# Kernel tuning notes

Measured on AMD Instinct MI355X. Metric: run time of the kernel, lower is better.

The kernel has to match this reference:

```python
import jax, jax.numpy as jnp
import numpy as np

NUM_HEADS = 16
NHID = 64
D = NUM_HEADS * NHID  # 1024, also keys/query/values dim and out_dim
SL, BS = 2048, 32


def setup_inputs() -> dict:
    key = jax.random.key(0)
    ks = jax.random.split(key, 7)
    s = 1.0 / np.sqrt(D)
    return {
        "query": jax.random.normal(ks[0], (BS, D), jnp.float32),
        "keys": jax.random.normal(ks[1], (SL, BS, D), jnp.float32),
        "values": jax.random.normal(ks[2], (SL, BS, D), jnp.float32),
        "Wq": jax.random.normal(ks[3], (D, D), jnp.float32) * s,
        "Wk": jax.random.normal(ks[4], (D, D), jnp.float32) * s,
        "Wv": jax.random.normal(ks[5], (D, D), jnp.float32) * s,
        "Wo": jax.random.normal(ks[6], (D, D), jnp.float32) * s,
    }


def reference(query, keys, values, Wq, Wk, Wv, Wo):
    sl, bs, _ = keys.shape
    qp = query @ Wq.T                       # [bs, H*nhid]
    kp = keys @ Wk.T                        # [sl, bs, H*nhid]
    vp = values @ Wv.T                      # [sl, bs, H*nhid]
    # elementwise multiplicative score, reduced per head
    dot = (qp * kp).reshape(sl, bs, NUM_HEADS, NHID).sum(-1) / np.sqrt(NHID)
    # NOTE: original uses log_softmax (not softmax) over the sequence dim
    w = jax.nn.log_softmax(dot, axis=0)[..., None]        # [sl, bs, H, 1]
    attn = (w * vp.reshape(sl, bs, NUM_HEADS, NHID)).sum(0)  # [bs, H, nhid]
    return attn.reshape(bs, -1) @ Wo.T                     # [bs, D]
```

## Files before the change

### kernel.cpp

```cpp
#include <hip/hip_runtime.h>

#define SL  2048
#define BSZ 32
#define DIM 1024
#define NH  16
#define HD  64

typedef __attribute__((ext_vector_type(4))) float f32x4;
typedef __attribute__((ext_vector_type(8))) short s16x8;

static __device__ __forceinline__ short f2bf(float f) {
    union { float f; unsigned u; } v; v.f = f;
    unsigned r = (v.u + 0x7fffu + ((v.u >> 16) & 1u)) >> 16;
    return (short)r;
}

__global__ __launch_bounds__(256) void k_qu(const float* __restrict__ query,
                                            const float* __restrict__ Wq,
                                            const float* __restrict__ Wk,
                                            short* __restrict__ u) {
    int b = blockIdx.x & 31;
    int h = blockIdx.x >> 5;
    int t = threadIdx.x;
    __shared__ float red[256];
    __shared__ float sq[HD];
    {
        int i  = t >> 2;
        int kq = t & 3;
        const float* q = query + (size_t)b * DIM + kq * 256;
        const float* w = Wq + (size_t)(h * HD + i) * DIM + kq * 256;
        f32x4 acc = {0.f, 0.f, 0.f, 0.f};
#pragma unroll 4
        for (int k = 0; k < 256; k += 4)
            acc += *(const f32x4*)(q + k) * *(const f32x4*)(w + k);
        red[t] = acc[0] + acc[1] + acc[2] + acc[3];
    }
    __syncthreads();
    if (t < HD) sq[t] = (red[t*4] + red[t*4+1] + red[t*4+2] + red[t*4+3]) * 0.125f;
    __syncthreads();
    f32x4 acc = {0.f, 0.f, 0.f, 0.f};
    const float* wk = Wk + (size_t)(h * HD) * DIM;
#pragma unroll 8
    for (int i = 0; i < HD; ++i) {
        float s = sq[i];
        const float* row = wk + (size_t)i * DIM;
        acc[0] += s * row[t];
        acc[1] += s * row[t + 256];
        acc[2] += s * row[t + 512];
        acc[3] += s * row[t + 768];
    }
    short* ub = u + ((size_t)(b * NH + h)) * DIM;
    ub[t]       = f2bf(acc[0]);
    ub[t + 256] = f2bf(acc[1]);
    ub[t + 512] = f2bf(acc[2]);
    ub[t + 768] = f2bf(acc[3]);
}

__global__ __launch_bounds__(256) void k_dot2(const float* __restrict__ keys,
                                              const short* __restrict__ u,
                                              float* __restrict__ dot,
                                              float2* __restrict__ part) {
    int b  = blockIdx.x & 31;
    int st = blockIdx.x >> 5;
    int s0 = st * 16;
    __shared__ short ulds[NH][DIM + 8];
    __shared__ short klds[16][DIM + 8];
    __shared__ f32x4 redc[4][64];
    int t = threadIdx.x;
    int w = t >> 6, l = t & 63;

    {
        const uint4* src = (const uint4*)(u + (size_t)b * NH * DIM);
        for (int idx = t; idx < NH * DIM / 8; idx += 256) {
            int row = idx >> 7;
            int col = (idx & 127) * 8;
            *(uint4*)&ulds[row][col] = src[idx];
        }
    }
#pragma unroll
    for (int r = 0; r < 4; ++r) {
        int srow = w * 4 + r;
        const float* kr = keys + ((size_t)(s0 + srow) * BSZ + b) * DIM;
#pragma unroll
        for (int kq = 0; kq < 4; ++kq) {
            f32x4 v = *(const f32x4*)(kr + kq * 256 + l * 4);
            ushort4 o;
            o.x = (unsigned short)f2bf(v[0]);
            o.y = (unsigned short)f2bf(v[1]);
            o.z = (unsigned short)f2bf(v[2]);
            o.w = (unsigned short)f2bf(v[3]);
            *(ushort4*)&klds[srow][kq * 256 + l * 4] = o;
        }
    }
    __syncthreads();

    int lrow = l & 15, kgrp = l >> 4;
    f32x4 acc = {0.f, 0.f, 0.f, 0.f};
#pragma unroll
    for (int kk = 0; kk < 8; ++kk) {
        int kj = w * 256 + kk * 32 + kgrp * 8;
        s16x8 af = *(const s16x8*)&klds[lrow][kj];
        s16x8 bf = *(const s16x8*)&ulds[lrow][kj];
        acc = __builtin_amdgcn_mfma_f32_16x16x32_bf16(af, bf, acc, 0, 0, 0);
    }
    redc[w][l] = acc;
    __syncthreads();
    if (t < 64) {
        f32x4 sum = redc[0][t] + redc[1][t] + redc[2][t] + redc[3][t];
        int lr = t & 15, kg = t >> 4;
        size_t obase = ((size_t)b * SL + (s0 + kg * 4)) * NH + lr;
#pragma unroll
        for (int r = 0; r < 4; ++r)
            dot[obase + (size_t)r * NH] = sum[r];
        float m = fmaxf(fmaxf(sum[0], sum[1]), fmaxf(sum[2], sum[3]));
        m = fmaxf(m, __shfl_xor(m, 16));
        m = fmaxf(m, __shfl_xor(m, 32));
        float lsum = __expf(sum[0]-m) + __expf(sum[1]-m) + __expf(sum[2]-m) + __expf(sum[3]-m);
        lsum += __shfl_xor(lsum, 16);
        lsum += __shfl_xor(lsum, 32);
        if (t < 16)
            part[((size_t)b * 128 + st) * 16 + t] = make_float2(m, lsum);
    }
}

__global__ __launch_bounds__(512) void k_zpart(const float* __restrict__ values,
                                               const float* __restrict__ dotb,
                                               float* __restrict__ zpart,
                                               float* __restrict__ svpart) {
    int b  = blockIdx.x & 31;
    int sq = blockIdx.x >> 5;
    int t  = threadIdx.x;
    __shared__ f32x4 wlds4[1024];
    {
        const f32x4* src = (const f32x4*)(dotb + ((size_t)b * SL + sq * 256) * NH);
        wlds4[t]       = src[t];
        wlds4[t + 512] = src[t + 512];
    }
    __syncthreads();
    const float* wlds = (const float*)wlds4;

    float ax[NH], ay[NH];
#pragma unroll
    for (int h = 0; h < NH; ++h) { ax[h] = 0.f; ay[h] = 0.f; }
    float svx = 0.f, svy = 0.f;

    const float* vbase = values + ((size_t)(sq * 256) * BSZ + b) * DIM + t * 2;
#pragma unroll 8
    for (int s = 0; s < 256; ++s) {
        float2 v = *(const float2*)(vbase + (size_t)s * (BSZ * DIM));
        const float* wr = wlds + s * 16;
#pragma unroll
        for (int h = 0; h < NH; ++h) {
            float wh = wr[h];
            ax[h] += v.x * wh;
            ay[h] += v.y * wh;
        }
        svx += v.x;
        svy += v.y;
    }
    float* zp = zpart + (size_t)(sq * 32 + b) * NH * DIM + t * 2;
#pragma unroll
    for (int h = 0; h < NH; ++h) {
        float2 o; o.x = ax[h]; o.y = ay[h];
        *(float2*)(zp + (size_t)h * DIM) = o;
    }
    float2 sv; sv.x = svx; sv.y = svy;
    *(float2*)(svpart + (size_t)(sq * 32 + b) * DIM + t * 2) = sv;
}

__global__ __launch_bounds__(256) void k_attn(const float* __restrict__ zpart,
                                              const float* __restrict__ svpart,
                                              const float2* __restrict__ part,
                                              const float* __restrict__ Wv,
                                              float* __restrict__ attn) {
    int oc = blockIdx.x & 15;
    int b  = blockIdx.x >> 4;
    int t  = threadIdx.x;
    int wv = t >> 6, l = t & 63;
    __shared__ float mred[16][16], lred[16][16];
    __shared__ float Tl[16];
    __shared__ float arow[DIM];
    __shared__ float red[4][64];
    {
        int h = t & 15, g = t >> 4;
        const float2* pb = part + (size_t)b * 128 * 16 + h;
        float M = -1e30f;
        float2 ps[8];
#pragma unroll
        for (int i = 0; i < 8; ++i) ps[i] = pb[(size_t)(g * 8 + i) * 16];
#pragma unroll
        for (int i = 0; i < 8; ++i) M = fmaxf(M, ps[i].x);
        float L = 0.f;
#pragma unroll
        for (int i = 0; i < 8; ++i) L += ps[i].y * __expf(ps[i].x - M);
        mred[g][h] = M; lred[g][h] = L;
    }
    __syncthreads();
    if (t < 16) {
        float M = mred[0][t];
#pragma unroll
        for (int g = 1; g < 16; ++g) M = fmaxf(M, mred[g][t]);
        float L = 0.f;
#pragma unroll
        for (int g = 0; g < 16; ++g) L += lred[g][t] * __expf(mred[g][t] - M);
        Tl[t] = M + __logf(L);
    }
    __syncthreads();
    {
        int k = wv * 256 + l * 4;
        f32x4 a = {0.f,0.f,0.f,0.f}, sv = {0.f,0.f,0.f,0.f};
#pragma unroll
        for (int p = 0; p < 8; ++p) {
            a  += *(const f32x4*)(zpart + ((size_t)((p * 32 + b) * NH + oc)) * DIM + k);
            sv += *(const f32x4*)(svpart + (size_t)(p * 32 + b) * DIM + k);
        }
        a -= Tl[oc] * sv;
        *(f32x4*)&arow[k] = a;
    }
    __syncthreads();
    const float* wr = Wv + (size_t)(oc * 64 + l) * DIM + wv * 256;
    const float* ar = arow + wv * 256;
    f32x4 acc = {0.f,0.f,0.f,0.f};
#pragma unroll 4
    for (int kk = 0; kk < 256; kk += 4)
        acc += *(const f32x4*)(ar + kk) * *(const f32x4*)(wr + kk);
    red[wv][l] = acc[0] + acc[1] + acc[2] + acc[3];
    __syncthreads();
    if (t < 64)
        attn[(size_t)b * DIM + oc * 64 + t] = red[0][t] + red[1][t] + red[2][t] + red[3][t];
}

__global__ __launch_bounds__(256) void k_out(const float* __restrict__ A,
                                             const float* __restrict__ W,
                                             float* __restrict__ O) {
    int oc = blockIdx.x & 15;
    int b  = blockIdx.x >> 4;
    int wv = __builtin_amdgcn_readfirstlane(threadIdx.x >> 6);
    int l  = threadIdx.x & 63;
    int o  = oc * 64 + l;
    const float* arow = A + (size_t)b * DIM + wv * 256;
    const float* wrow = W + (size_t)o * DIM + wv * 256;
    f32x4 acc = {0.f, 0.f, 0.f, 0.f};
#pragma unroll 4
    for (int k = 0; k < 256; k += 4) {
        f32x4 a = *(const f32x4*)(arow + k);
        f32x4 w = *(const f32x4*)(wrow + k);
        acc += a * w;
    }
    __shared__ float red[4][64];
    red[wv][l] = acc[0] + acc[1] + acc[2] + acc[3];
    __syncthreads();
    int t = threadIdx.x;
    if (t < 64)
        O[(size_t)b * DIM + oc * 64 + t] = red[0][t] + red[1][t] + red[2][t] + red[3][t];
}

extern "C" void kernel_launch(void* const* d_in, const int* in_sizes, int n_in,
                              void* d_out, int out_size, void* d_ws, size_t ws_size,
                              hipStream_t stream) {
    const float* query  = (const float*)d_in[0];
    const float* keys   = (const float*)d_in[1];
    const float* values = (const float*)d_in[2];
    const float* Wq = (const float*)d_in[3];
    const float* Wk = (const float*)d_in[4];
    const float* Wv = (const float*)d_in[5];
    const float* Wo = (const float*)d_in[6];
    float* out = (float*)d_out;

    char* ws = (char*)d_ws;
    short*  u      = (short*)(ws + 0);
    float*  dotb   = (float*)(ws + (1 << 20));
    float2* part   = (float2*)(ws + (5 << 20));
    float*  zpart  = (float*)(ws + (5 << 20) + (512 << 10));
    float*  svpart = (float*)(ws + (21 << 20) + (512 << 10));
    float*  attn   = (float*)(ws + (22 << 20) + (512 << 10));

    hipLaunchKernelGGL(k_qu,    dim3(512),  dim3(256), 0, stream, query, Wq, Wk, u);
    hipLaunchKernelGGL(k_dot2,  dim3(4096), dim3(256), 0, stream, keys, u, dotb, part);
    hipLaunchKernelGGL(k_zpart, dim3(256),  dim3(512), 0, stream, values, dotb, zpart, svpart);
    hipLaunchKernelGGL(k_attn,  dim3(512),  dim3(256), 0, stream, zpart, svpart, part, Wv, attn);
    hipLaunchKernelGGL(k_out,   dim3(512),  dim3(256), 0, stream, attn, Wo, out);
}
```

Measured before the change: 212.3 us.

## Batch four rows per block in small GEMV kernels to reuse weights

k_qu, k_attn and k_out now process four batch rows per block, so each weight row is loaded once and applied to four activation vectors. The grids shrink from 512 to 128 blocks. The log-sum-exp combine in k_attn becomes a wave shuffle reduction, and k_zpart reads its LDS weights as float4 vectors. This trades parallelism, with fewer blocks than CUs, for lower weight bandwidth.

Result: slower. 230.4 us (+8.6%).

```diff
diff --git a/kernel.cpp b/kernel.cpp
--- a/kernel.cpp
+++ b/kernel.cpp
@@ -19,41 +19,69 @@
                                             const float* __restrict__ Wq,
                                             const float* __restrict__ Wk,
                                             short* __restrict__ u) {
-    int b = blockIdx.x & 31;
-    int h = blockIdx.x >> 5;
+    int h  = blockIdx.x >> 3;
+    int bg = blockIdx.x & 7;
+    int b0 = bg * 4;
     int t = threadIdx.x;
-    __shared__ float red[256];
-    __shared__ float sq[HD];
-    {
-        int i  = t >> 2;
-        int kq = t & 3;
-        const float* q = query + (size_t)b * DIM + kq * 256;
-        const float* w = Wq + (size_t)(h * HD + i) * DIM + kq * 256;
-        f32x4 acc = {0.f, 0.f, 0.f, 0.f};
+    __shared__ float qlds[4][DIM];
+    __shared__ float red[4][64][4];
+    __shared__ float sq[4][HD];
+
+#pragma unroll
+    for (int r = 0; r < 4; ++r) {
+        int idx = t + r * 256;
+        int kk = (idx & 255) * 4;
+        *(f32x4*)&qlds[r][kk] = *(const f32x4*)(query + (size_t)(b0 + r) * DIM + kk);
+    }
+    __syncthreads();
+    {
+        int i = t & 63, kq = t >> 6;
+        const float* wrow = Wq + (size_t)(h * HD + i) * DIM + kq * 256;
+        const float* q0 = &qlds[0][kq * 256];
+        const float* q1 = &qlds[1][kq * 256];
+        const float* q2 = &qlds[2][kq * 256];
+        const float* q3 = &qlds[3][kq * 256];
+        f32x4 a0 = {0,0,0,0}, a1 = {0,0,0,0}, a2 = {0,0,0,0}, a3 = {0,0,0,0};
 #pragma unroll 4
-        for (int k = 0; k < 256; k += 4)
-            acc += *(const f32x4*)(q + k) * *(const f32x4*)(w + k);
-        red[t] = acc[0] + acc[1] + acc[2] + acc[3];
-    }
-    __syncthreads();
-    if (t < HD) sq[t] = (red[t*4] + red[t*4+1] + red[t*4+2] + red[t*4+3]) * 0.125f;
-    __syncthreads();
-    f32x4 acc = {0.f, 0.f, 0.f, 0.f};
-    const float* wk = Wk + (size_t)(h * HD) * DIM;
+        for (int k = 0; k < 256; k += 4) {
+            f32x4 wv = *(const f32x4*)(wrow + k);
+            a0 += wv * *(const f32x4*)(q0 + k);
+            a1 += wv * *(const f32x4*)(q1 + k);
+            a2 += wv * *(const f32x4*)(q2 + k);
+            a3 += wv * *(const f32x4*)(q3 + k);
+        }
+        red[kq][i][0] = a0[0]+a0[1]+a0[2]+a0[3];
+        red[kq][i][1] = a1[0]+a1[1]+a1[2]+a1[3];
+        red[kq][i][2] = a2[0]+a2[1]+a2[2]+a2[3];
+        red[kq][i][3] = a3[0]+a3[1]+a3[2]+a3[3];
+    }
+    __syncthreads();
+    {
+        int bb = t & 3, i = t >> 2;
+        sq[bb][i] = (red[0][i][bb] + red[1][i][bb] + red[2][i][bb] + red[3][i][bb]) * 0.125f;
+    }
+    __syncthreads();
+    f32x4 acc[4];
+#pragma unroll
+    for (int bb = 0; bb < 4; ++bb) acc[bb] = (f32x4){0,0,0,0};
+    const float* wk = Wk + (size_t)(h * HD) * DIM + t * 4;
 #pragma unroll 8
     for (int i = 0; i < HD; ++i) {
-        float s = sq[i];
-        const float* row = wk + (size_t)i * DIM;
-        acc[0] += s * row[t];
-        acc[1] += s * row[t + 256];
-        acc[2] += s * row[t + 512];
-        acc[3] += s * row[t + 768];
-    }
-    short* ub = u + ((size_t)(b * NH + h)) * DIM;
-    ub[t]       = f2bf(acc[0]);
-    ub[t + 256] = f2bf(acc[1]);
-    ub[t + 512] = f2bf(acc[2]);
-    ub[t + 768] = f2bf(acc[3]);
+        f32x4 wv = *(const f32x4*)(wk + (size_t)i * DIM);
+        acc[0] += sq[0][i] * wv;
+        acc[1] += sq[1][i] * wv;
+        acc[2] += sq[2][i] * wv;
+        acc[3] += sq[3][i] * wv;
+    }
+#pragma unroll
+    for (int bb = 0; bb < 4; ++bb) {
+        ushort4 o;
+        o.x = (unsigned short)f2bf(acc[bb][0]);
+        o.y = (unsigned short)f2bf(acc[bb][1]);
+        o.z = (unsigned short)f2bf(acc[bb][2]);
+        o.w = (unsigned short)f2bf(acc[bb][3]);
+        *(ushort4*)(u + ((size_t)((b0 + bb) * NH + h)) * DIM + t * 4) = o;
+    }
 }
 
 __global__ __launch_bounds__(256) void k_dot2(const float* __restrict__ keys,
@@ -137,7 +165,6 @@
         wlds4[t + 512] = src[t + 512];
     }
     __syncthreads();
-    const float* wlds = (const float*)wlds4;
 
     float ax[NH], ay[NH];
 #pragma unroll
@@ -148,15 +175,25 @@
 #pragma unroll 8
     for (int s = 0; s < 256; ++s) {
         float2 v = *(const float2*)(vbase + (size_t)s * (BSZ * DIM));
-        const float* wr = wlds + s * 16;
-#pragma unroll
-        for (int h = 0; h < NH; ++h) {
-            float wh = wr[h];
-            ax[h] += v.x * wh;
-            ay[h] += v.y * wh;
-        }
-        svx += v.x;
-        svy += v.y;
+        const f32x4* wr = wlds4 + s * 4;
+        f32x4 w0 = wr[0], w1 = wr[1], w2 = wr[2], w3 = wr[3];
+        ax[0]  += v.x * w0[0]; ay[0]  += v.y * w0[0];
+        ax[1]  += v.x * w0[1]; ay[1]  += v.y * w0[1];
+        ax[2]  += v.x * w0[2]; ay[2]  += v.y * w0[2];
+        ax[3]  += v.x * w0[3]; ay[3]  += v.y * w0[3];
+        ax[4]  += v.x * w1[0]; ay[4]  += v.y * w1[0];
+        ax[5]  += v.x * w1[1]; ay[5]  += v.y * w1[1];
+        ax[6]  += v.x * w1[2]; ay[6]  += v.y * w1[2];
+        ax[7]  += v.x * w1[3]; ay[7]  += v.y * w1[3];
+        ax[8]  += v.x * w2[0]; ay[8]  += v.y * w2[0];
+        ax[9]  += v.x * w2[1]; ay[9]  += v.y * w2[1];
+        ax[10] += v.x * w2[2]; ay[10] += v.y * w2[2];
+        ax[11] += v.x * w2[3]; ay[11] += v.y * w2[3];
+        ax[12] += v.x * w3[0]; ay[12] += v.y * w3[0];
+        ax[13] += v.x * w3[1]; ay[13] += v.y * w3[1];
+        ax[14] += v.x * w3[2]; ay[14] += v.y * w3[2];
+        ax[15] += v.x * w3[3]; ay[15] += v.y * w3[3];
+        svx += v.x; svy += v.y;
     }
     float* zp = zpart + (size_t)(sq * 32 + b) * NH * DIM + t * 2;
 #pragma unroll
@@ -173,86 +210,70 @@
                                               const float2* __restrict__ part,
                                               const float* __restrict__ Wv,
                                               float* __restrict__ attn) {
-    int oc = blockIdx.x & 15;
-    int b  = blockIdx.x >> 4;
-    int t  = threadIdx.x;
-    int wv = t >> 6, l = t & 63;
-    __shared__ float mred[16][16], lred[16][16];
-    __shared__ float Tl[16];
-    __shared__ float arow[DIM];
-    __shared__ float red[4][64];
-    {
-        int h = t & 15, g = t >> 4;
-        const float2* pb = part + (size_t)b * 128 * 16 + h;
-        float M = -1e30f;
-        float2 ps[8];
-#pragma unroll
-        for (int i = 0; i < 8; ++i) ps[i] = pb[(size_t)(g * 8 + i) * 16];
-#pragma unroll
-        for (int i = 0; i < 8; ++i) M = fmaxf(M, ps[i].x);
-        float L = 0.f;
-#pragma unroll
-        for (int i = 0; i < 8; ++i) L += ps[i].y * __expf(ps[i].x - M);
-        mred[g][h] = M; lred[g][h] = L;
-    }
-    __syncthreads();
-    if (t < 16) {
-        float M = mred[0][t];
-#pragma unroll
-        for (int g = 1; g < 16; ++g) M = fmaxf(M, mred[g][t]);
-        float L = 0.f;
-#pragma unroll
-        for (int g = 0; g < 16; ++g) L += lred[g][t] * __expf(mred[g][t] - M);
-        Tl[t] = M + __logf(L);
-    }
-    __syncthreads();
-    {
-        int k = wv * 256 + l * 4;
-        f32x4 a = {0.f,0.f,0.f,0.f}, sv = {0.f,0.f,0.f,0.f};
+    int oc = blockIdx.x >> 3;
+    int bg = blockIdx.x & 7;
+    int t = threadIdx.x, w = t >> 6, l = t & 63;
+    int b = bg * 4 + w;
+    __shared__ float arow[4][DIM];
+
+    float T;
+    {
+        const float2* pb = part + ((size_t)b * 128) * 16 + oc;
+        float2 p0 = pb[(size_t)l * 16];
+        float2 p1 = pb[(size_t)(l + 64) * 16];
+        float M = fmaxf(p0.x, p1.x);
+        float L = p0.y * __expf(p0.x - M) + p1.y * __expf(p1.x - M);
+#pragma unroll
+        for (int off = 1; off < 64; off <<= 1) {
+            float oM = __shfl_xor(M, off);
+            float oL = __shfl_xor(L, off);
+            float nm = fmaxf(M, oM);
+            L = L * __expf(M - nm) + oL * __expf(oM - nm);
+            M = nm;
+        }
+        T = M + __logf(L);
+    }
+#pragma unroll
+    for (int kq = 0; kq < 4; ++kq) {
+        int k = kq * 256 + l * 4;
+        f32x4 a = {0,0,0,0}, sv = {0,0,0,0};
 #pragma unroll
         for (int p = 0; p < 8; ++p) {
             a  += *(const f32x4*)(zpart + ((size_t)((p * 32 + b) * NH + oc)) * DIM + k);
             sv += *(const f32x4*)(svpart + (size_t)(p * 32 + b) * DIM + k);
         }
-        a -= Tl[oc] * sv;
-        *(f32x4*)&arow[k] = a;
-    }
-    __syncthreads();
-    const float* wr = Wv + (size_t)(oc * 64 + l) * DIM + wv * 256;
-    const float* ar = arow + wv * 256;
-    f32x4 acc = {0.f,0.f,0.f,0.f};
+        a -= T * sv;
+        *(f32x4*)&arow[w][k] = a;
+    }
+    const float* wrow = Wv + (size_t)(oc * 64 + l) * DIM;
+    const float* ar = arow[w];
+    f32x4 acc = {0,0,0,0};
 #pragma unroll 4
-    for (int kk = 0; kk < 256; kk += 4)
-        acc += *(const f32x4*)(ar + kk) * *(const f32x4*)(wr + kk);
-    red[wv][l] = acc[0] + acc[1] + acc[2] + acc[3];
-    __syncthreads();
-    if (t < 64)
-        attn[(size_t)b * DIM + oc * 64 + t] = red[0][t] + red[1][t] + red[2][t] + red[3][t];
+    for (int k = 0; k < DIM; k += 4)
+        acc += *(const f32x4*)(ar + k) * *(const f32x4*)(wrow + k);
+    attn[(size_t)b * DIM + oc * 64 + l] = acc[0] + acc[1] + acc[2] + acc[3];
 }
 
 __global__ __launch_bounds__(256) void k_out(const float* __restrict__ A,
                                              const float* __restrict__ W,
                                              float* __restrict__ O) {
-    int oc = blockIdx.x & 15;
-    int b  = blockIdx.x >> 4;
-    int wv = __builtin_amdgcn_readfirstlane(threadIdx.x >> 6);
-    int l  = threadIdx.x & 63;
-    int o  = oc * 64 + l;
-    const float* arow = A + (size_t)b * DIM + wv * 256;
-    const float* wrow = W + (size_t)o * DIM + wv * 256;
-    f32x4 acc = {0.f, 0.f, 0.f, 0.f};
+    int oc = blockIdx.x >> 3;
+    int bg = blockIdx.x & 7;
+    int t = threadIdx.x, w = t >> 6, l = t & 63;
+    int b = bg * 4 + w;
+    __shared__ float arow[4][DIM];
+#pragma unroll
+    for (int kq = 0; kq < 4; ++kq) {
+        int k = kq * 256 + l * 4;
+        *(f32x4*)&arow[w][k] = *(const f32x4*)(A + (size_t)b * DIM + k);
+    }
+    const float* wrow = W + (size_t)(oc * 64 + l) * DIM;
+    const float* ar = arow[w];
+    f32x4 acc = {0,0,0,0};
 #pragma unroll 4
-    for (int k = 0; k < 256; k += 4) {
-        f32x4 a = *(const f32x4*)(arow + k);
-        f32x4 w = *(const f32x4*)(wrow + k);
-        acc += a * w;
-    }
-    __shared__ float red[4][64];
-    red[wv][l] = acc[0] + acc[1] + acc[2] + acc[3];
-    __syncthreads();
-    int t = threadIdx.x;
-    if (t < 64)
-        O[(size_t)b * DIM + oc * 64 + t] = red[0][t] + red[1][t] + red[2][t] + red[3][t];
+    for (int k = 0; k < DIM; k += 4)
+        acc += *(const f32x4*)(ar + k) * *(const f32x4*)(wrow + k);
+    O[(size_t)b * DIM + oc * 64 + l] = acc[0] + acc[1] + acc[2] + acc[3];
 }
 
 extern "C" void kernel_launch(void* const* d_in, const int* in_sizes, int n_in,
@@ -275,9 +296,9 @@
     float*  svpart = (float*)(ws + (21 << 20) + (512 << 10));
     float*  attn   = (float*)(ws + (22 << 20) + (512 << 10));
 
-    hipLaunchKernelGGL(k_qu,    dim3(512),  dim3(256), 0, stream, query, Wq, Wk, u);
+    hipLaunchKernelGGL(k_qu,    dim3(128),  dim3(256), 0, stream, query, Wq, Wk, u);
     hipLaunchKernelGGL(k_dot2,  dim3(4096), dim3(256), 0, stream, keys, u, dotb, part);
     hipLaunchKernelGGL(k_zpart, dim3(256),  dim3(512), 0, stream, values, dotb, zpart, svpart);
-    hipLaunchKernelGGL(k_attn,  dim3(512),  dim3(256), 0, stream, zpart, svpart, part, Wv, attn);
-    hipLaunchKernelGGL(k_out,   dim3(512),  dim3(256), 0, stream, attn, Wo, out);
-}
+    hipLaunchKernelGGL(k_attn,  dim3(128),  dim3(256), 0, stream, zpart, svpart, part, Wv, attn);
+    hipLaunchKernelGGL(k_out,   dim3(128),  dim3(256), 0, stream, attn, Wo, out);
+}
```
